# Kernel optimization log

Measured on AMD Instinct MI355X. Metric: run time of the kernel, lower is better.

Reference implementation:

```python
import jax, jax.numpy as jnp
import numpy as np

CH = 128
GROUPS = 8
HEADS = 8
HEAD_DIM = CH // HEADS  # 16
EPS = 1e-5


def setup_inputs() -> dict:
    key = jax.random.key(0)
    ks = jax.random.split(key, 5)
    x = jax.random.normal(ks[0], (8, CH, 128, 128), dtype=jnp.float32)
    gn_w = jnp.ones((CH,), dtype=jnp.float32)
    gn_b = jnp.zeros((CH,), dtype=jnp.float32)
    w_in = jax.random.normal(ks[1], (CH, CH), dtype=jnp.float32) * (1.0 / np.sqrt(CH))
    b_in = jax.random.normal(ks[2], (CH,), dtype=jnp.float32) * 0.01
    w_out = jax.random.normal(ks[3], (CH, CH), dtype=jnp.float32) * (1.0 / np.sqrt(CH))
    b_out = jax.random.normal(ks[4], (CH,), dtype=jnp.float32) * 0.01
    return {"x": x, "gn_w": gn_w, "gn_b": gn_b, "w_in": w_in, "b_in": b_in,
            "w_out": w_out, "b_out": b_out}


def _group_norm(x, gamma, beta):
    b, c, H, W = x.shape
    xg = x.reshape(b, GROUPS, c // GROUPS, H, W)
    mean = xg.mean(axis=(2, 3, 4), keepdims=True)
    var = xg.var(axis=(2, 3, 4), keepdims=True)
    xg = (xg - mean) * jax.lax.rsqrt(var + EPS)
    x = xg.reshape(b, c, H, W)
    return x * gamma[None, :, None, None] + beta[None, :, None, None]


def _conv1x1(x, w, bias):
    # w: [out_c, in_c] (1x1 conv == pointwise matmul over channels)
    return jnp.einsum('oc,bchw->bohw', w, x) + bias[None, :, None, None]


def reference(x, gn_w, gn_b, w_in, b_in, w_out, b_out):
    b, c, H, W = x.shape
    h = _group_norm(x, gn_w, gn_b)
    h = _conv1x1(h, w_in, b_in)
    # reshape to [b, heads, head_dim, H*W]; attention over head_dim axis,
    # contracting the spatial axis (d = H*W) as in the original einsums
    hh = h.reshape(b, HEADS, HEAD_DIM, H * W)
    scale = HEAD_DIM ** (-0.5)
    scores = jnp.einsum('bhid,bhjd->bhij', hh, hh) * scale  # [b,heads,hd,hd]
    weights = jax.nn.softmax(scores, axis=-1)
    attn = jnp.einsum('bhij,bhjd->bhid', weights, hh)
    attn = attn.reshape(b, c, H, W)
    h = _conv1x1(attn, w_out, b_out)
    return x + h
```

## Files before the change

kernel.cpp:

```cpp
#include <hip/hip_runtime.h>


#define NPOS 16384

typedef short short8 __attribute__((ext_vector_type(8)));
typedef float f32x4 __attribute__((ext_vector_type(4)));

__device__ __forceinline__ unsigned short f2bf(float f) {
    union { float f; unsigned u; } v; v.f = f;
    unsigned r = (v.u + 0x7fffu + ((v.u >> 16) & 1u)) >> 16;
    return (unsigned short)r;
}

__global__ __launch_bounds__(512, 2) void k_gram(const float* __restrict__ x,
                                                 float* __restrict__ Gpart,
                                                 float* __restrict__ mpart) {
    __shared__ __align__(16) unsigned char SH[69632];

    const int t = threadIdx.x;
    const int lane = t & 63, wv = t >> 6;
    const int q = lane >> 4, i16 = lane & 15;
    const int blk = blockIdx.x;
    const int b = blk >> 5, slab = blk & 31;
    const size_t d0 = (size_t)slab << 9;

    f32x4 acc[8];
    f32x4 macc = (f32x4){0.f, 0.f, 0.f, 0.f};
#pragma unroll
    for (int ct = 0; ct < 8; ++ct) acc[ct] = (f32x4){0.f, 0.f, 0.f, 0.f};
    const short8 ones = {(short)0x3F80, (short)0x3F80, (short)0x3F80, (short)0x3F80,
                         (short)0x3F80, (short)0x3F80, (short)0x3F80, (short)0x3F80};
    const float* xb = x + (size_t)b * (128 * NPOS) + d0;
    unsigned short* Xs = (unsigned short*)SH;
    const int r0 = wv * 16 + i16;

    for (int cc = 0; cc < 2; ++cc) {
        if (cc) __syncthreads();
#pragma unroll
        for (int i = 0; i < 16; ++i) {
            int idx = t + i * 512;
            int c = idx >> 6, d4 = idx & 63;
            float4 v = *((const float4*)(xb + (size_t)c * NPOS + cc * 256) + d4);
            ushort4 o;
            o.x = f2bf(v.x); o.y = f2bf(v.y); o.z = f2bf(v.z); o.w = f2bf(v.w);
            int g = d4 >> 1;
            int sg = g ^ (c & 7);
            *(ushort4*)&Xs[c * 256 + (sg << 3) + ((d4 & 1) << 2)] = o;
        }
        __syncthreads();
#pragma unroll
        for (int ks = 0; ks < 8; ++ks) {
            int gd = ks * 4 + q;
            short8 af = *(const short8*)&Xs[r0 * 256 + ((gd ^ (r0 & 7)) << 3)];
            macc = __builtin_amdgcn_mfma_f32_16x16x32_bf16(af, ones, macc, 0, 0, 0);
#pragma unroll
            for (int ct = 0; ct < 8; ++ct) {
                int rb = ct * 16 + i16;
                short8 bb = *(const short8*)&Xs[rb * 256 + ((gd ^ (rb & 7)) << 3)];
                acc[ct] = __builtin_amdgcn_mfma_f32_16x16x32_bf16(af, bb, acc[ct], 0, 0, 0);
            }
        }
    }
    if (i16 == 0) {
#pragma unroll
        for (int r = 0; r < 4; ++r)
            mpart[blk * 128 + wv * 16 + q * 4 + r] = macc[r];
    }
    __syncthreads();

    float* Tf = (float*)SH;
#pragma unroll
    for (int ct = 0; ct < 8; ++ct)
#pragma unroll
        for (int r = 0; r < 4; ++r)
            Tf[(wv * 16 + q * 4 + r) * 132 + ct * 16 + i16] = acc[ct][r];
    __syncthreads();
    float4* gp = (float4*)(Gpart + (size_t)blk * 16384);
#pragma unroll
    for (int i = 0; i < 8; ++i) {
        int fi = t + i * 512;
        int row = fi >> 5, c4 = fi & 31;
        gp[row * 32 + c4] = *(float4*)&Tf[row * 132 + c4 * 4];
    }
}

__global__ __launch_bounds__(256) void k_reduce(const float* __restrict__ Gpart,
                                                const float* __restrict__ mpart,
                                                float* __restrict__ G,
                                                float* __restrict__ mv) {
    int t = threadIdx.x;
    int fi = blockIdx.x * 256 + t;
    int b = fi >> 12, off4 = fi & 4095;
    const float4* Gp4 = (const float4*)Gpart;
    float4 s = (float4){0.f, 0.f, 0.f, 0.f};
#pragma unroll 8
    for (int sl = 0; sl < 32; ++sl) {
        float4 v = Gp4[(size_t)(b * 32 + sl) * 4096 + off4];
        s.x += v.x; s.y += v.y; s.z += v.z; s.w += v.w;
    }
    ((float4*)G)[fi] = s;
    if (blockIdx.x < 8 && t < 128) {
        float ms = 0.f;
#pragma unroll 8
        for (int sl = 0; sl < 32; ++sl) ms += mpart[(blockIdx.x * 32 + sl) * 128 + t];
        mv[blockIdx.x * 128 + t] = ms;
    }
}

__global__ __launch_bounds__(512, 1) void k_fold(
    const float* __restrict__ G, const float* __restrict__ mvG,
    const float* __restrict__ gn_w, const float* __restrict__ gn_b,
    const float* __restrict__ w_in, const float* __restrict__ b_in,
    const float* __restrict__ w_out, const float* __restrict__ b_out,
    unsigned short* __restrict__ Mb, float* __restrict__ bias2) {
    __shared__ unsigned short As[128 * 136];
    __shared__ unsigned short At[128 * 136];
    __shared__ unsigned short Ts[128 * 136];
    __shared__ float sW[2048];
    __shared__ float sm[128], ss[128], st[128], sv[128], su[128];
    __shared__ float red[8][128];

    const int t = threadIdx.x;
    const int lane = t & 63, wv = t >> 6;
    const int q = lane >> 4, i16 = lane & 15;
    const int b = blockIdx.x;
    const float* Gb = G + b * 16384;

    if (t < 128) sm[t] = mvG[b * 128 + t];
    __syncthreads();
    if (t < 128) {
        int g = t >> 4;
        float s1 = 0.f, s2 = 0.f;
#pragma unroll
        for (int k = 0; k < 16; ++k) {
            int c = g * 16 + k;
            s1 += sm[c];
            s2 += Gb[c * 128 + c];
        }
        const float invN = 1.0f / 262144.0f;
        float mean = s1 * invN;
        float var = s2 * invN - mean * mean;
        float rstd = rsqrtf(var + 1e-5f);
        float s = gn_w[t] * rstd;
        ss[t] = s;
        st[t] = gn_b[t] - mean * s;
    }
    __syncthreads();

    {
        int c = t & 127, quarter = t >> 7;
        float v = 0.f, u = 0.f;
        const float* wr = w_in + c * 128 + quarter * 32;
        unsigned short* ar = &As[c * 136 + quarter * 32];
#pragma unroll
        for (int k = 0; k < 32; ++k) {
            int kg = quarter * 32 + k;
            float w = wr[k];
            float a = w * ss[kg];
            unsigned short ab = f2bf(a);
            ar[k] = ab;
            At[kg * 136 + c] = ab;
            v += w * st[kg];
            u += a * sm[kg];
        }
        red[quarter][c] = v;
        red[4 + quarter][c] = u;
    }
    for (int idx = t; idx < 16384; idx += 512)
        Ts[(idx >> 7) * 136 + (idx & 127)] = f2bf(Gb[idx]);
    __syncthreads();
    if (t < 128) {
        sv[t] = b_in[t] + red[0][t] + red[1][t] + red[2][t] + red[3][t];
        su[t] = red[4][t] + red[5][t] + red[6][t] + red[7][t];
    }
    __syncthreads();

    f32x4 tacc[8];
#pragma unroll
    for (int ct = 0; ct < 8; ++ct) tacc[ct] = (f32x4){0.f, 0.f, 0.f, 0.f};
    const int rA = wv * 16 + i16;
#pragma unroll
    for (int ks = 0; ks < 4; ++ks) {
        short8 af = *(const short8*)&As[rA * 136 + ks * 32 + q * 8];
#pragma unroll
        for (int ct = 0; ct < 8; ++ct) {
            short8 gbf = *(const short8*)&Ts[(ct * 16 + i16) * 136 + ks * 32 + q * 8];
            tacc[ct] = __builtin_amdgcn_mfma_f32_16x16x32_bf16(af, gbf, tacc[ct], 0, 0, 0);
        }
    }
    __syncthreads();
#pragma unroll
    for (int ct = 0; ct < 8; ++ct)
#pragma unroll
        for (int r = 0; r < 4; ++r)
            Ts[(wv * 16 + q * 4 + r) * 136 + ct * 16 + i16] = f2bf(tacc[ct][r]);
    __syncthreads();

    {
        f32x4 sacc = (f32x4){0.f, 0.f, 0.f, 0.f};
#pragma unroll
        for (int ks = 0; ks < 4; ++ks) {
            short8 tf = *(const short8*)&Ts[rA * 136 + ks * 32 + q * 8];
            short8 af = *(const short8*)&As[rA * 136 + ks * 32 + q * 8];
            sacc = __builtin_amdgcn_mfma_f32_16x16x32_bf16(tf, af, sacc, 0, 0, 0);
        }
        int J = wv * 16 + i16;
        float vJ = sv[J], uJ = su[J];
#pragma unroll
        for (int r = 0; r < 4; ++r) {
            int I = wv * 16 + q * 4 + r;
            float val = (sacc[r] + su[I] * vJ + sv[I] * uJ + 16384.f * sv[I] * vJ) * 0.25f;
            float mx = val;
#pragma unroll
            for (int msk = 1; msk < 16; msk <<= 1) mx = fmaxf(mx, __shfl_xor(mx, msk));
            float e = __expf(val - mx);
            float sum = e;
#pragma unroll
            for (int msk = 1; msk < 16; msk <<= 1) sum += __shfl_xor(sum, msk);
            sW[I * 16 + i16] = e / sum;
        }
    }
    __syncthreads();

    {
        int c = t & 127, grp = t >> 7;
        unsigned short* Ps = Ts;
        float pb = 0.f;
#pragma unroll
        for (int hh = 0; hh < 2; ++hh) {
            int h = grp * 2 + hh;
            float wrow[16];
#pragma unroll
            for (int i = 0; i < 16; ++i) wrow[i] = w_out[c * 128 + h * 16 + i];
#pragma unroll
            for (int j = 0; j < 16; ++j) {
                float val = 0.f;
#pragma unroll
                for (int i = 0; i < 16; ++i) val += wrow[i] * sW[(h * 16 + i) * 16 + j];
                Ps[c * 136 + h * 16 + j] = f2bf(val);
                pb += val * sv[h * 16 + j];
            }
        }
        red[grp][c] = pb;
    }
    __syncthreads();
    if (t < 128)
        bias2[b * 128 + t] = b_out[t] + red[0][t] + red[1][t] + red[2][t] + red[3][t];

    {
        f32x4 macc[8];
#pragma unroll
        for (int ct = 0; ct < 8; ++ct) macc[ct] = (f32x4){0.f, 0.f, 0.f, 0.f};
#pragma unroll
        for (int ks = 0; ks < 4; ++ks) {
            short8 pf = *(const short8*)&Ts[rA * 136 + ks * 32 + q * 8];
#pragma unroll
            for (int ct = 0; ct < 8; ++ct) {
                short8 atf = *(const short8*)&At[(ct * 16 + i16) * 136 + ks * 32 + q * 8];
                macc[ct] = __builtin_amdgcn_mfma_f32_16x16x32_bf16(pf, atf, macc[ct], 0, 0, 0);
            }
        }
        unsigned short* mb = Mb + (size_t)b * 16384;
#pragma unroll
        for (int ct = 0; ct < 8; ++ct)
#pragma unroll
            for (int r = 0; r < 4; ++r)
                mb[(wv * 16 + q * 4 + r) * 128 + ct * 16 + i16] = f2bf(macc[ct][r]);
    }
}

__global__ __launch_bounds__(256, 4) void k_out(const float* __restrict__ x,
                                                const unsigned short* __restrict__ Mb,
                                                const float* __restrict__ bias2,
                                                float* __restrict__ out) {
    __shared__ unsigned short Xt[128 * 128];
    __shared__ float b2s[128];

    const int t = threadIdx.x;
    const int lane = t & 63, wv = t >> 6;
    const int q = lane >> 4, i16 = lane & 15;
    const int b = blockIdx.x >> 7;
    const int p0 = (blockIdx.x & 127) << 7;

    if (t < 128) b2s[t] = bias2[b * 128 + t];

    const float* xb = x + (size_t)b * (128 * NPOS) + p0;
#pragma unroll
    for (int i = 0; i < 16; ++i) {
        int p = ((i & 1) << 6) + lane;
        int kq = (wv << 3) + (i >> 1);
        const float* col = xb + (size_t)(kq * 4) * NPOS + p;
        float a0 = col[0];
        float a1 = col[NPOS];
        float a2 = col[2 * NPOS];
        float a3 = col[3 * NPOS];
        ushort4 o; o.x = f2bf(a0); o.y = f2bf(a1); o.z = f2bf(a2); o.w = f2bf(a3);
        int g = kq >> 1;
        int sg = g ^ (p & 7);
        *(ushort4*)&Xt[p * 128 + (sg << 3) + ((kq & 1) << 2)] = o;
    }
    __syncthreads();

    f32x4 acc[2][8];
#pragma unroll
    for (int a = 0; a < 2; ++a)
#pragma unroll
        for (int pt = 0; pt < 8; ++pt) acc[a][pt] = (f32x4){0.f, 0.f, 0.f, 0.f};

    const unsigned short* Mrow = Mb + (size_t)b * 16384;
#pragma unroll
    for (int ks = 0; ks < 4; ++ks) {
        short8 a0 = *(const short8*)&Mrow[(wv * 32 + i16) * 128 + ks * 32 + q * 8];
        short8 a1 = *(const short8*)&Mrow[(wv * 32 + 16 + i16) * 128 + ks * 32 + q * 8];
        int g = ks * 4 + q;
#pragma unroll
        for (int pt = 0; pt < 8; ++pt) {
            int pr = pt * 16 + i16;
            short8 bb = *(const short8*)&Xt[pr * 128 + ((g ^ (pr & 7)) << 3)];
            acc[0][pt] = __builtin_amdgcn_mfma_f32_16x16x32_bf16(a0, bb, acc[0][pt], 0, 0, 0);
            acc[1][pt] = __builtin_amdgcn_mfma_f32_16x16x32_bf16(a1, bb, acc[1][pt], 0, 0, 0);
        }
    }

    float* ob = out + (size_t)b * (128 * NPOS) + p0;
#pragma unroll
    for (int a = 0; a < 2; ++a) {
        int cb = wv * 32 + a * 16 + q * 4;
#pragma unroll
        for (int pt = 0; pt < 8; ++pt) {
            int p = pt * 16 + i16;
#pragma unroll
            for (int r = 0; r < 4; ++r) {
                int c = cb + r;
                ob[(size_t)c * NPOS + p] = acc[a][pt][r] + b2s[c] + xb[(size_t)c * NPOS + p];
            }
        }
    }
}

extern "C" void kernel_launch(void* const* d_in, const int* in_sizes, int n_in,
                              void* d_out, int out_size, void* d_ws, size_t ws_size,
                              hipStream_t stream) {
    const float* x    = (const float*)d_in[0];
    const float* gn_w = (const float*)d_in[1];
    const float* gn_b = (const float*)d_in[2];
    const float* w_in = (const float*)d_in[3];
    const float* b_in = (const float*)d_in[4];
    const float* w_out= (const float*)d_in[5];
    const float* b_out= (const float*)d_in[6];
    float* out = (float*)d_out;

    char* ws = (char*)d_ws;
    float* Gpart          = (float*)(ws + 0);
    float* mpart          = (float*)(ws + 16777216);
    float* G              = (float*)(ws + 16908288);
    float* mvG            = (float*)(ws + 17432576);
    float* bias2          = (float*)(ws + 17436672);
    unsigned short* Mb    = (unsigned short*)(ws + 17440768);

    k_gram<<<dim3(256), dim3(512), 0, stream>>>(x, Gpart, mpart);
    k_reduce<<<dim3(128), dim3(256), 0, stream>>>(Gpart, mpart, G, mvG);
    k_fold<<<dim3(8), dim3(512), 0, stream>>>(G, mvG, gn_w, gn_b, w_in, b_in,
                                              w_out, b_out, Mb, bias2);
    k_out<<<dim3(1024), dim3(256), 0, stream>>>(x, Mb, bias2, out);
}
```

Baseline: 168.7 us.

## Fuse gram, reduce and fold kernels with inter-block flag synchronization

Merges the Gram-partial, reduction and fold kernels into one persistent kernel. Blocks publish per-block flags after writing partials, wait for the other blocks of their batch, do a distributed reduction straight to bf16, then block slab 0 of each batch waits again and runs the fold. This removes two kernel launches and the fp32 reduced Gram round trip. In exchange it relies on all 256 blocks being co-resident (occupancy lowered to 1 block per CU with larger LDS) and on spin-waits, which risks deadlock and leaves the fold serialized on 8 blocks.

```diff
diff --git a/kernel.cpp b/kernel.cpp
--- a/kernel.cpp
+++ b/kernel.cpp
@@ -2,6 +2,8 @@
 
 
 #define NPOS 16384
+#define MAGA 0xA11C0DE5u
+#define MAGB 0xB22C0DE5u
 
 typedef short short8 __attribute__((ext_vector_type(8)));
 typedef float f32x4 __attribute__((ext_vector_type(4)));
@@ -12,10 +14,17 @@
     return (unsigned short)r;
 }
 
-__global__ __launch_bounds__(512, 2) void k_gram(const float* __restrict__ x,
-                                                 float* __restrict__ Gpart,
-                                                 float* __restrict__ mpart) {
-    __shared__ __align__(16) unsigned char SH[69632];
+__global__ __launch_bounds__(512, 1) void k_gramfold(
+    const float* __restrict__ x,
+    const float* __restrict__ gn_w, const float* __restrict__ gn_b,
+    const float* __restrict__ w_in, const float* __restrict__ b_in,
+    const float* __restrict__ w_out, const float* __restrict__ b_out,
+    float* Gpart, float* mpart,
+    unsigned int* flagA, unsigned int* flagB,
+    unsigned short* Gbf, float* Gdiag,
+    unsigned short* __restrict__ Mb, float* __restrict__ bias2) {
+
+    __shared__ __align__(16) unsigned char SH[119296];
 
     const int t = threadIdx.x;
     const int lane = t & 63, wv = t >> 6;
@@ -24,110 +33,124 @@
     const int b = blk >> 5, slab = blk & 31;
     const size_t d0 = (size_t)slab << 9;
 
-    f32x4 acc[8];
-    f32x4 macc = (f32x4){0.f, 0.f, 0.f, 0.f};
-#pragma unroll
-    for (int ct = 0; ct < 8; ++ct) acc[ct] = (f32x4){0.f, 0.f, 0.f, 0.f};
-    const short8 ones = {(short)0x3F80, (short)0x3F80, (short)0x3F80, (short)0x3F80,
-                         (short)0x3F80, (short)0x3F80, (short)0x3F80, (short)0x3F80};
-    const float* xb = x + (size_t)b * (128 * NPOS) + d0;
-    unsigned short* Xs = (unsigned short*)SH;
-    const int r0 = wv * 16 + i16;
-
-    for (int cc = 0; cc < 2; ++cc) {
-        if (cc) __syncthreads();
-#pragma unroll
-        for (int i = 0; i < 16; ++i) {
-            int idx = t + i * 512;
-            int c = idx >> 6, d4 = idx & 63;
-            float4 v = *((const float4*)(xb + (size_t)c * NPOS + cc * 256) + d4);
-            ushort4 o;
-            o.x = f2bf(v.x); o.y = f2bf(v.y); o.z = f2bf(v.z); o.w = f2bf(v.w);
-            int g = d4 >> 1;
-            int sg = g ^ (c & 7);
-            *(ushort4*)&Xs[c * 256 + (sg << 3) + ((d4 & 1) << 2)] = o;
+    {
+        unsigned short* Xs = (unsigned short*)SH;
+        f32x4 acc[8];
+        f32x4 macc = (f32x4){0.f, 0.f, 0.f, 0.f};
+#pragma unroll
+        for (int ct = 0; ct < 8; ++ct) acc[ct] = (f32x4){0.f, 0.f, 0.f, 0.f};
+        const short8 ones = {(short)0x3F80, (short)0x3F80, (short)0x3F80, (short)0x3F80,
+                             (short)0x3F80, (short)0x3F80, (short)0x3F80, (short)0x3F80};
+        const float* xb = x + (size_t)b * (128 * NPOS) + d0;
+        const int r0 = wv * 16 + i16;
+
+        for (int cc = 0; cc < 2; ++cc) {
+            if (cc) __syncthreads();
+#pragma unroll
+            for (int i = 0; i < 16; ++i) {
+                int idx = t + i * 512;
+                int c = idx >> 6, d4 = idx & 63;
+                float4 v = *((const float4*)(xb + (size_t)c * NPOS + cc * 256) + d4);
+                ushort4 o;
+                o.x = f2bf(v.x); o.y = f2bf(v.y); o.z = f2bf(v.z); o.w = f2bf(v.w);
+                int g = d4 >> 1;
+                int sg = g ^ (c & 7);
+                *(ushort4*)&Xs[c * 256 + (sg << 3) + ((d4 & 1) << 2)] = o;
+            }
+            __syncthreads();
+#pragma unroll
+            for (int ks = 0; ks < 8; ++ks) {
+                int gd = ks * 4 + q;
+                short8 af = *(const short8*)&Xs[r0 * 256 + ((gd ^ (r0 & 7)) << 3)];
+                macc = __builtin_amdgcn_mfma_f32_16x16x32_bf16(af, ones, macc, 0, 0, 0);
+#pragma unroll
+                for (int ct = 0; ct < 8; ++ct) {
+                    int rb = ct * 16 + i16;
+                    short8 bb = *(const short8*)&Xs[rb * 256 + ((gd ^ (rb & 7)) << 3)];
+                    acc[ct] = __builtin_amdgcn_mfma_f32_16x16x32_bf16(af, bb, acc[ct], 0, 0, 0);
+                }
+            }
+        }
+        if (i16 == 0) {
+#pragma unroll
+            for (int r = 0; r < 4; ++r)
+                mpart[blk * 128 + wv * 16 + q * 4 + r] = macc[r];
         }
         __syncthreads();
-#pragma unroll
-        for (int ks = 0; ks < 8; ++ks) {
-            int gd = ks * 4 + q;
-            short8 af = *(const short8*)&Xs[r0 * 256 + ((gd ^ (r0 & 7)) << 3)];
-            macc = __builtin_amdgcn_mfma_f32_16x16x32_bf16(af, ones, macc, 0, 0, 0);
-#pragma unroll
-            for (int ct = 0; ct < 8; ++ct) {
-                int rb = ct * 16 + i16;
-                short8 bb = *(const short8*)&Xs[rb * 256 + ((gd ^ (rb & 7)) << 3)];
-                acc[ct] = __builtin_amdgcn_mfma_f32_16x16x32_bf16(af, bb, acc[ct], 0, 0, 0);
-            }
-        }
-    }
-    if (i16 == 0) {
-#pragma unroll
-        for (int r = 0; r < 4; ++r)
-            mpart[blk * 128 + wv * 16 + q * 4 + r] = macc[r];
-    }
-    __syncthreads();
-
-    float* Tf = (float*)SH;
-#pragma unroll
-    for (int ct = 0; ct < 8; ++ct)
-#pragma unroll
-        for (int r = 0; r < 4; ++r)
-            Tf[(wv * 16 + q * 4 + r) * 132 + ct * 16 + i16] = acc[ct][r];
-    __syncthreads();
-    float4* gp = (float4*)(Gpart + (size_t)blk * 16384);
-#pragma unroll
-    for (int i = 0; i < 8; ++i) {
-        int fi = t + i * 512;
-        int row = fi >> 5, c4 = fi & 31;
-        gp[row * 32 + c4] = *(float4*)&Tf[row * 132 + c4 * 4];
-    }
-}
-
-__global__ __launch_bounds__(256) void k_reduce(const float* __restrict__ Gpart,
-                                                const float* __restrict__ mpart,
-                                                float* __restrict__ G,
-                                                float* __restrict__ mv) {
-    int t = threadIdx.x;
-    int fi = blockIdx.x * 256 + t;
-    int b = fi >> 12, off4 = fi & 4095;
-    const float4* Gp4 = (const float4*)Gpart;
-    float4 s = (float4){0.f, 0.f, 0.f, 0.f};
+
+        float* Tf = (float*)SH;
+#pragma unroll
+        for (int ct = 0; ct < 8; ++ct)
+#pragma unroll
+            for (int r = 0; r < 4; ++r)
+                Tf[(wv * 16 + q * 4 + r) * 132 + ct * 16 + i16] = acc[ct][r];
+        __syncthreads();
+        float4* gp = (float4*)(Gpart + (size_t)blk * 16384);
+#pragma unroll
+        for (int i = 0; i < 8; ++i) {
+            int fi = t + i * 512;
+            int row = fi >> 5, c4 = fi & 31;
+            gp[row * 32 + c4] = *(float4*)&Tf[row * 132 + c4 * 4];
+        }
+    }
+    __threadfence();
+    __syncthreads();
+    if (t == 0) atomicExch(&flagA[blk], MAGA ^ (unsigned)blk);
+
+    if (t < 32) {
+        unsigned exp = MAGA ^ (unsigned)(b * 32 + t);
+        while (atomicAdd(&flagA[b * 32 + t], 0u) != exp) __builtin_amdgcn_s_sleep(2);
+    }
+    __syncthreads();
+    __threadfence();
+
+    float* sm = (float*)(SH + 112640);
+    if (t < 128) {
+        int off4 = slab * 128 + t;
+        const float4* Gp4 = (const float4*)Gpart;
+        float4 s = (float4){0.f, 0.f, 0.f, 0.f};
 #pragma unroll 8
-    for (int sl = 0; sl < 32; ++sl) {
-        float4 v = Gp4[(size_t)(b * 32 + sl) * 4096 + off4];
-        s.x += v.x; s.y += v.y; s.z += v.z; s.w += v.w;
-    }
-    ((float4*)G)[fi] = s;
-    if (blockIdx.x < 8 && t < 128) {
+        for (int sl = 0; sl < 32; ++sl) {
+            float4 v = Gp4[(size_t)(b * 32 + sl) * 4096 + off4];
+            s.x += v.x; s.y += v.y; s.z += v.z; s.w += v.w;
+        }
+        int row = slab * 4 + (t >> 5);
+        int col = (t & 31) * 4;
+        ushort4 o;
+        o.x = f2bf(s.x); o.y = f2bf(s.y); o.z = f2bf(s.z); o.w = f2bf(s.w);
+        *(ushort4*)&Gbf[b * 16384 + row * 128 + col] = o;
+        if ((t & 31) == slab)
+            Gdiag[b * 128 + row] = ((float*)&s)[t >> 5];
+    }
+    if (slab == 0 && t < 128) {
         float ms = 0.f;
 #pragma unroll 8
-        for (int sl = 0; sl < 32; ++sl) ms += mpart[(blockIdx.x * 32 + sl) * 128 + t];
-        mv[blockIdx.x * 128 + t] = ms;
-    }
-}
-
-__global__ __launch_bounds__(512, 1) void k_fold(
-    const float* __restrict__ G, const float* __restrict__ mvG,
-    const float* __restrict__ gn_w, const float* __restrict__ gn_b,
-    const float* __restrict__ w_in, const float* __restrict__ b_in,
-    const float* __restrict__ w_out, const float* __restrict__ b_out,
-    unsigned short* __restrict__ Mb, float* __restrict__ bias2) {
-    __shared__ unsigned short As[128 * 136];
-    __shared__ unsigned short At[128 * 136];
-    __shared__ unsigned short Ts[128 * 136];
-    __shared__ float sW[2048];
-    __shared__ float sm[128], ss[128], st[128], sv[128], su[128];
-    __shared__ float red[8][128];
-
-    const int t = threadIdx.x;
-    const int lane = t & 63, wv = t >> 6;
-    const int q = lane >> 4, i16 = lane & 15;
-    const int b = blockIdx.x;
-    const float* Gb = G + b * 16384;
-
-    if (t < 128) sm[t] = mvG[b * 128 + t];
-    __syncthreads();
+        for (int sl = 0; sl < 32; ++sl) ms += mpart[(b * 32 + sl) * 128 + t];
+        sm[t] = ms;
+    }
+    __threadfence();
+    __syncthreads();
+    if (t == 0) atomicExch(&flagB[blk], MAGB ^ (unsigned)blk);
+
+    if (slab != 0) return;
+
+    if (t < 32) {
+        unsigned exp = MAGB ^ (unsigned)(b * 32 + t);
+        while (atomicAdd(&flagB[b * 32 + t], 0u) != exp) __builtin_amdgcn_s_sleep(2);
+    }
+    __syncthreads();
+    __threadfence();
+
+    unsigned short* As = (unsigned short*)SH;
+    unsigned short* At = (unsigned short*)(SH + 34816);
+    unsigned short* Ts = (unsigned short*)(SH + 69632);
+    float* sW = (float*)(SH + 104448);
+    float* ss = (float*)(SH + 113152);
+    float* st = (float*)(SH + 113664);
+    float* sv = (float*)(SH + 114176);
+    float* su = (float*)(SH + 114688);
+    float* red = (float*)(SH + 115200);
+
     if (t < 128) {
         int g = t >> 4;
         float s1 = 0.f, s2 = 0.f;
@@ -135,7 +158,7 @@
         for (int k = 0; k < 16; ++k) {
             int c = g * 16 + k;
             s1 += sm[c];
-            s2 += Gb[c * 128 + c];
+            s2 += Gdiag[b * 128 + c];
         }
         const float invN = 1.0f / 262144.0f;
         float mean = s1 * invN;
@@ -163,15 +186,21 @@
             v += w * st[kg];
             u += a * sm[kg];
         }
-        red[quarter][c] = v;
-        red[4 + quarter][c] = u;
-    }
-    for (int idx = t; idx < 16384; idx += 512)
-        Ts[(idx >> 7) * 136 + (idx & 127)] = f2bf(Gb[idx]);
+        red[quarter * 128 + c] = v;
+        red[(4 + quarter) * 128 + c] = u;
+    }
+    {
+        const ushort4* gb4 = (const ushort4*)(Gbf + b * 16384);
+#pragma unroll
+        for (int i4 = t; i4 < 4096; i4 += 512) {
+            int row = i4 >> 5, c4 = i4 & 31;
+            *(ushort4*)&Ts[row * 136 + c4 * 4] = gb4[i4];
+        }
+    }
     __syncthreads();
     if (t < 128) {
-        sv[t] = b_in[t] + red[0][t] + red[1][t] + red[2][t] + red[3][t];
-        su[t] = red[4][t] + red[5][t] + red[6][t] + red[7][t];
+        sv[t] = b_in[t] + red[t] + red[128 + t] + red[256 + t] + red[384 + t];
+        su[t] = red[512 + t] + red[640 + t] + red[768 + t] + red[896 + t];
     }
     __syncthreads();
 
@@ -241,11 +270,11 @@
                 pb += val * sv[h * 16 + j];
             }
         }
-        red[grp][c] = pb;
+        red[grp * 128 + c] = pb;
     }
     __syncthreads();
     if (t < 128)
-        bias2[b * 128 + t] = b_out[t] + red[0][t] + red[1][t] + red[2][t] + red[3][t];
+        bias2[b * 128 + t] = b_out[t] + red[t] + red[128 + t] + red[256 + t] + red[384 + t];
 
     {
         f32x4 macc[8];
@@ -353,14 +382,16 @@
     char* ws = (char*)d_ws;
     float* Gpart          = (float*)(ws + 0);
     float* mpart          = (float*)(ws + 16777216);
-    float* G              = (float*)(ws + 16908288);
-    float* mvG            = (float*)(ws + 17432576);
-    float* bias2          = (float*)(ws + 17436672);
-    unsigned short* Mb    = (unsigned short*)(ws + 17440768);
-
-    k_gram<<<dim3(256), dim3(512), 0, stream>>>(x, Gpart, mpart);
-    k_reduce<<<dim3(128), dim3(256), 0, stream>>>(Gpart, mpart, G, mvG);
-    k_fold<<<dim3(8), dim3(512), 0, stream>>>(G, mvG, gn_w, gn_b, w_in, b_in,
-                                              w_out, b_out, Mb, bias2);
+    unsigned int* flagA   = (unsigned int*)(ws + 16908288);
+    unsigned int* flagB   = (unsigned int*)(ws + 16909312);
+    unsigned short* Gbf   = (unsigned short*)(ws + 16910336);
+    float* Gdiag          = (float*)(ws + 17172480);
+    float* bias2          = (float*)(ws + 17176576);
+    unsigned short* Mb    = (unsigned short*)(ws + 17180672);
+
+    k_gramfold<<<dim3(256), dim3(512), 0, stream>>>(x, gn_w, gn_b, w_in, b_in,
+                                                    w_out, b_out, Gpart, mpart,
+                                                    flagA, flagB, Gbf, Gdiag,
+                                                    Mb, bias2);
     k_out<<<dim3(1024), dim3(256), 0, stream>>>(x, Mb, bias2, out);
 }
```

New measurement: 307.5 us. 1.82x slower.
